# Optimization experiments

Measured on AMD Instinct MI355X. Metric: run time of the kernel, lower is better.

The kernel has to match this reference:

```python
import jax, jax.numpy as jnp
import numpy as np

EPS = 1e-5  # InstanceNorm3d default eps


def _conv3d(x, w, b):
    # x: [C, D, H, W]; w: [O, I, 3, 3, 3]; SAME padding (pw = k//2)
    y = jax.lax.conv_general_dilated(
        x[None], w, window_strides=(1, 1, 1), padding='SAME',
        dimension_numbers=('NCDHW', 'OIDHW', 'NCDHW'))[0]
    return y + b[:, None, None, None]


def _spade(x, ws, bs, wg, bg, wb, bb):
    # x: [C, D, H, W] single sample; per-class SPADE params
    mu = x.mean(axis=(1, 2, 3), keepdims=True)
    var = x.var(axis=(1, 2, 3), keepdims=True)  # biased var, as in InstanceNorm
    normalized = (x - mu) * jax.lax.rsqrt(var + EPS)
    actv = jax.nn.relu(_conv3d(x, ws, bs))
    gamma = _conv3d(actv, wg, bg)
    beta = _conv3d(actv, wb, bb)
    return normalized * (1.0 + gamma) + beta


def setup_inputs() -> dict:
    key = jax.random.key(0)
    ks = jax.random.split(key, 6)
    B, C, D = 8, 32, 48
    NC, NH = 4, 64  # num_classes, nhidden
    s = 0.05
    return {
        'x': jax.random.normal(ks[0], (B, C, D, D, D), jnp.float32),
        'y': jax.random.randint(ks[1], (B,), 0, NC),
        'Wshared': jax.random.normal(ks[2], (NC, NH, C, 3, 3, 3), jnp.float32) * s,
        'bshared': jnp.zeros((NC, NH), jnp.float32),
        'Wgamma': jax.random.normal(ks[3], (NC, C, NH, 3, 3, 3), jnp.float32) * s,
        'bgamma': jnp.zeros((NC, C), jnp.float32),
        'Wbeta': jax.random.normal(ks[4], (NC, C, NH, 3, 3, 3), jnp.float32) * s,
        'bbeta': jnp.zeros((NC, C), jnp.float32),
    }


def reference(x, y, Wshared, bshared, Wgamma, bgamma, Wbeta, bbeta):
    # Gather per-sample expert params by class index, then batch via vmap
    return jax.vmap(_spade)(x, Wshared[y], bshared[y], Wgamma[y], bgamma[y],
                            Wbeta[y], bbeta[y])
```

## Files before the change

kernel.cpp:

```cpp
#include <hip/hip_runtime.h>
#include <stdint.h>

#define V3 (48*48*48)
#define BATCH 8

typedef __bf16 bf16x8 __attribute__((ext_vector_type(8)));
typedef float  f32x4  __attribute__((ext_vector_type(4)));

__device__ __forceinline__ unsigned short f2bf(float f) {
  uint32_t u = __float_as_uint(f);
  u += 0x7fffu + ((u >> 16) & 1u);
  return (unsigned short)(u >> 16);
}

#define GLDS16(gp, lp)                                                         \
  __builtin_amdgcn_global_load_lds(                                            \
      (const __attribute__((address_space(1))) void*)(gp),                     \
      (__attribute__((address_space(3))) void*)(lp), 16, 0, 0)

__global__ __launch_bounds__(1024)
void stats_kernel(const float* __restrict__ x, float* __restrict__ mu,
                  float* __restrict__ rstd, float4* __restrict__ zpage) {
  if (blockIdx.x == 0 && threadIdx.x < 64) {
    float4 z; z.x = 0.f; z.y = 0.f; z.z = 0.f; z.w = 0.f;
    zpage[threadIdx.x] = z;
  }
  const int bc = blockIdx.x;
  const float4* p = reinterpret_cast<const float4*>(x + (size_t)bc * V3);
  float s = 0.f, s2 = 0.f;
  for (int i = threadIdx.x; i < V3 / 4; i += 1024) {
    float4 v = p[i];
    s  += (v.x + v.y) + (v.z + v.w);
    s2 += (v.x * v.x + v.y * v.y) + (v.z * v.z + v.w * v.w);
  }
  for (int o = 32; o; o >>= 1) { s += __shfl_down(s, o); s2 += __shfl_down(s2, o); }
  __shared__ float red[32];
  const int wave = threadIdx.x >> 6, lane = threadIdx.x & 63;
  if (lane == 0) { red[wave] = s; red[16 + wave] = s2; }
  __syncthreads();
  if (threadIdx.x == 0) {
    float S1 = 0.f, S2 = 0.f;
#pragma unroll
    for (int i = 0; i < 16; ++i) { S1 += red[i]; S2 += red[16 + i]; }
    float m = S1 / (float)V3;
    float var = S2 / (float)V3 - m * m;
    mu[bc] = m;
    rstd[bc] = rsqrtf(var + 1e-5f);
  }
}

__global__ __launch_bounds__(256)
void repack_kernel(const float* __restrict__ x, unsigned short* __restrict__ xcl) {
  const int bid = blockIdx.x;
  const int h = bid % 48;
  const int d = (bid / 48) % 48;
  const int b = bid / (48 * 48);
  __shared__ float tile[32][48];
  const float* src = x + (size_t)b * 32 * V3 + (size_t)(d * 48 + h) * 48;
  for (int i = threadIdx.x; i < 32 * 48; i += 256) {
    int c = i / 48, w = i - c * 48;
    tile[c][w] = src[(size_t)c * V3 + w];
  }
  __syncthreads();
  const int i = threadIdx.x;
  if (i < 48 * 4) {
    const int w = i >> 2, pp = i & 3;
    alignas(16) unsigned short pk[8];
#pragma unroll
    for (int j = 0; j < 8; ++j) pk[j] = f2bf(tile[pp * 8 + j][w]);
    *reinterpret_cast<uint4*>(
        &xcl[((size_t)b * V3 + (size_t)(d * 48 + h) * 48 + w) * 32 + pp * 8]) =
        *reinterpret_cast<const uint4*>(pk);
  }
}

__global__ __launch_bounds__(256)
void wprep_kernel(const int* __restrict__ y, const float* __restrict__ Wsh,
                  const float* __restrict__ Wg, const float* __restrict__ Wb,
                  unsigned short* __restrict__ w1, unsigned short* __restrict__ w23) {
  const int N1 = BATCH * 27 * 4 * 64 * 8;
  const int N2 = BATCH * 2 * 27 * 4 * 64 * 8;
  int idx = blockIdx.x * 256 + threadIdx.x;
  if (idx < N1) {
    const int j = idx & 7;
    const int lane = (idx >> 3) & 63;
    const int mt = (idx >> 9) & 3;
    const int tap = (idx >> 11) % 27;
    const int b = idx / (27 << 11);
    const int q = lane >> 4, n = lane & 15;
    const int cout = mt * 16 + n, cin = q * 8 + j;
    const int cls = y[b];
    w1[idx] = f2bf(Wsh[((size_t)((cls * 64 + cout) * 32 + cin)) * 27 + tap]);
  } else if (idx < N1 + N2) {
    const int t = idx - N1;
    const int b = t / 110592;
    const int r1 = t - b * 110592;
    const int kc = r1 / 55296;
    const int r2 = r1 - kc * 55296;
    const int tap = r2 >> 11;
    const int r3 = r2 & 2047;
    const int mt = r3 >> 9;
    const int lane = (r3 >> 3) & 63;
    const int j = r3 & 7;
    const int q = lane >> 4, n = lane & 15;
    const int cout = mt * 16 + n, cin = kc * 32 + q * 8 + j;
    const int cls = y[b];
    float v = (cout < 32) ? Wg[((size_t)((cls * 32 + cout) * 64 + cin)) * 27 + tap]
                          : Wb[((size_t)((cls * 32 + (cout - 32)) * 64 + cin)) * 27 + tap];
    w23[t] = f2bf(v);
  }
}


#define STAGE_K(K0, K1, SRC_EXPR)                                              \
  do {                                                                         \
    _Pragma("unroll") for (int k = (K0); k < (K1); ++k) {                      \
      const int j = tid + k * 256;                                             \
      if (k < 10 || tid < 32) {                                                \
        const int ld_ = j / 432;                                               \
        const int r = j - ld_ * 432;                                           \
        const int pp = r / 108;                                                \
        const int r2 = r - pp * 108;                                           \
        const int lh = r2 / 18;                                                \
        const int lw = r2 - lh * 18;                                           \
        const int d = d0 + ld_ - 1, h = h0 + lh - 1, w = w0 + lw - 1;          \
        const bool ok = (unsigned)d < 48u && (unsigned)h < 48u && (unsigned)w < 48u; \
        const void* gp = ok ? (const void*)(SRC_EXPR)                          \
                            : (const void*)((const char*)zpage + lane * 16);   \
        GLDS16(gp, &lds[(size_t)(j - lane) * 8]);                              \
      }                                                                        \
    }                                                                          \
  } while (0)

#define STAGE11(SRC_EXPR)                                                      \
  do {                                                                         \
    STAGE_K(0, 7, SRC_EXPR);                                                   \
    __builtin_amdgcn_sched_barrier(0);         \
    STAGE_K(7, 11, SRC_EXPR);                                                  \
  } while (0)

#define WAIT_VM(N)                                                             \
  asm volatile("s_waitcnt vmcnt(" #N ")" ::: "memory")

#define COMPUTE_TAPS_PF(T0, T1, WB)                                            \
  do {                                                                         \
    __builtin_amdgcn_s_setprio(1);                                             \
    _Pragma("unroll 1") for (int tap = (T0); tap < (T1); ++tap) {              \
      bf16x8 anxt[4];                                                          \
      _Pragma("unroll") for (int mt = 0; mt < 4; ++mt)                         \
        anxt[mt] = *reinterpret_cast<const bf16x8*>(                           \
            &(WB)[((tap + 1) * 4 + mt) * 512]);                                \
      const int dz_ = tap / 9, rr_ = tap - dz_ * 9;                            \
      const int dy_ = rr_ / 3, dx_ = rr_ - dy_ * 3;                            \
      const int vb_ = ((wave + dz_) * 4 + q) * 108 + dy_ * 18 + dx_ + n;       \
      bf16x8 bf[4];                                                            \
      _Pragma("unroll") for (int g = 0; g < 4; ++g)                            \
        bf[g] = *reinterpret_cast<const bf16x8*>(&lds[(size_t)(vb_ + g * 18) * 8]); \
      _Pragma("unroll") for (int g = 0; g < 4; ++g)                            \
        _Pragma("unroll") for (int mt = 0; mt < 4; ++mt)                       \
          acc[g][mt] = __builtin_amdgcn_mfma_f32_16x16x32_bf16(                \
              acur[mt], bf[g], acc[g][mt], 0, 0, 0);                           \
      _Pragma("unroll") for (int mt = 0; mt < 4; ++mt) acur[mt] = anxt[mt];    \
    }                                                                          \
    __builtin_amdgcn_s_setprio(0);                                             \
  } while (0)

#define COMPUTE_TAP26()                                                        \
  do {                                                                         \
    __builtin_amdgcn_s_setprio(1);                                             \
    const int vb_ = ((wave + 2) * 4 + q) * 108 + 2 * 18 + 2 + n;               \
    bf16x8 bf[4];                                                              \
    _Pragma("unroll") for (int g = 0; g < 4; ++g)                              \
      bf[g] = *reinterpret_cast<const bf16x8*>(&lds[(size_t)(vb_ + g * 18) * 8]); \
    _Pragma("unroll") for (int g = 0; g < 4; ++g)                              \
      _Pragma("unroll") for (int mt = 0; mt < 4; ++mt)                         \
        acc[g][mt] = __builtin_amdgcn_mfma_f32_16x16x32_bf16(                  \
            acur[mt], bf[g], acc[g][mt], 0, 0, 0);                             \
    __builtin_amdgcn_s_setprio(0);                                             \
  } while (0)

__global__ __launch_bounds__(256, 3)
void conv1_kernel(const unsigned short* __restrict__ xcl,
                  const unsigned short* __restrict__ w1,
                  const int* __restrict__ y, const float* __restrict__ bsh,
                  unsigned short* __restrict__ actv,
                  const float4* __restrict__ zpage) {
  const int d0 = (blockIdx.y / 12) * 4;
  const int h0 = (blockIdx.y % 12) * 4;
  const int w0 = blockIdx.x * 16;
  const int b = blockIdx.z;

  __shared__ unsigned short lds[2592 * 8];

  const int tid = threadIdx.x;
  const int lane = tid & 63;
  const int wave = tid >> 6;
  const int q = lane >> 4, n = lane & 15;

  const unsigned short* xb = xcl + (size_t)b * V3 * 32;
  STAGE11(xb + ((size_t)((d * 48 + h) * 48 + w)) * 32 + pp * 8);

  const unsigned short* wb = w1 + (size_t)b * 55296 + lane * 8;
  bf16x8 acur[4];
#pragma unroll
  for (int mt = 0; mt < 4; ++mt)
    acur[mt] = *reinterpret_cast<const bf16x8*>(&wb[mt * 512]);
  __builtin_amdgcn_sched_barrier(0);

  f32x4 acc[4][4];
#pragma unroll
  for (int g = 0; g < 4; ++g)
#pragma unroll
    for (int mt = 0; mt < 4; ++mt) acc[g][mt] = (f32x4){0.f, 0.f, 0.f, 0.f};

  WAIT_VM(7);
  __builtin_amdgcn_s_barrier();
  COMPUTE_TAPS_PF(0, 9, wb);
  WAIT_VM(4);
  __builtin_amdgcn_s_barrier();
  COMPUTE_TAPS_PF(9, 26, wb);
  COMPUTE_TAP26();

  const int cls = y[b];
  const int od = d0 + wave, ow = w0 + n;
#pragma unroll
  for (int g = 0; g < 4; ++g) {
    const int oh = h0 + g;
    const size_t vg = (size_t)(od * 48 + oh) * 48 + ow;
#pragma unroll
    for (int mt = 0; mt < 4; ++mt) {
      const int c0 = mt * 16 + q * 4;
      ushort4 pk;
      pk.x = f2bf(fmaxf(acc[g][mt][0] + bsh[cls * 64 + c0 + 0], 0.f));
      pk.y = f2bf(fmaxf(acc[g][mt][1] + bsh[cls * 64 + c0 + 1], 0.f));
      pk.z = f2bf(fmaxf(acc[g][mt][2] + bsh[cls * 64 + c0 + 2], 0.f));
      pk.w = f2bf(fmaxf(acc[g][mt][3] + bsh[cls * 64 + c0 + 3], 0.f));
      *reinterpret_cast<ushort4*>(&actv[((size_t)b * V3 + vg) * 64 + c0]) = pk;
    }
  }
}

__global__ __launch_bounds__(256, 3)
void conv2_kernel(const unsigned short* __restrict__ actv,
                  const unsigned short* __restrict__ w23,
                  const int* __restrict__ y, const float* __restrict__ bgm,
                  const float* __restrict__ bbt, const float* __restrict__ x,
                  const float* __restrict__ mu, const float* __restrict__ rstd,
                  float* __restrict__ out, const float4* __restrict__ zpage) {
  const int d0 = (blockIdx.y / 12) * 4;
  const int h0 = (blockIdx.y % 12) * 4;
  const int w0 = blockIdx.x * 16;
  const int b = blockIdx.z;

  __shared__ unsigned short lds[2592 * 8];

  const int tid = threadIdx.x;
  const int lane = tid & 63;
  const int wave = tid >> 6;
  const int q = lane >> 4, n = lane & 15;

  f32x4 acc[4][4];
#pragma unroll
  for (int g = 0; g < 4; ++g)
#pragma unroll
    for (int mt = 0; mt < 4; ++mt) acc[g][mt] = (f32x4){0.f, 0.f, 0.f, 0.f};

  const unsigned short* ab = actv + (size_t)b * V3 * 64;

  for (int kc = 0; kc < 2; ++kc) {
    if (kc) { __syncthreads(); }
    STAGE11(ab + ((size_t)((d * 48 + h) * 48 + w)) * 64 + kc * 32 + pp * 8);

    const unsigned short* wb =
        w23 + (size_t)b * 110592 + (size_t)kc * 55296 + lane * 8;
    bf16x8 acur[4];
#pragma unroll
    for (int mt = 0; mt < 4; ++mt)
      acur[mt] = *reinterpret_cast<const bf16x8*>(&wb[mt * 512]);
    __builtin_amdgcn_sched_barrier(0);

    WAIT_VM(7);
    __builtin_amdgcn_s_barrier();
    COMPUTE_TAPS_PF(0, 9, wb);
    WAIT_VM(4);
    __builtin_amdgcn_s_barrier();
    COMPUTE_TAPS_PF(9, 26, wb);
    COMPUTE_TAP26();
  }

  const int cls = y[b];
  const int od = d0 + wave, ow = w0 + n;
#pragma unroll
  for (int g = 0; g < 4; ++g) {
    const int oh = h0 + g;
    const size_t vg = (size_t)(od * 48 + oh) * 48 + ow;
#pragma unroll
    for (int mt = 0; mt < 2; ++mt) {
#pragma unroll
      for (int r = 0; r < 4; ++r) {
        const int c = mt * 16 + q * 4 + r;
        const float gamma = acc[g][mt][r] + bgm[cls * 32 + c];
        const float beta = acc[g][mt + 2][r] + bbt[cls * 32 + c];
        const size_t xi = (size_t)(b * 32 + c) * V3 + vg;
        const float xn = (x[xi] - mu[b * 32 + c]) * rstd[b * 32 + c];
        out[xi] = xn * (1.f + gamma) + beta;
      }
    }
  }
}

extern "C" void kernel_launch(void* const* d_in, const int* in_sizes, int n_in,
                              void* d_out, int out_size, void* d_ws, size_t ws_size,
                              hipStream_t stream) {
  const float* x = (const float*)d_in[0];
  const int* y = (const int*)d_in[1];
  const float* Wsh = (const float*)d_in[2];
  const float* bsh = (const float*)d_in[3];
  const float* Wg = (const float*)d_in[4];
  const float* bg = (const float*)d_in[5];
  const float* Wb = (const float*)d_in[6];
  const float* bb = (const float*)d_in[7];
  float* out = (float*)d_out;

  char* ws = (char*)d_ws;
  unsigned short* xcl  = (unsigned short*)(ws + 0);
  unsigned short* actv = (unsigned short*)(ws + 56623104);
  unsigned short* w1   = (unsigned short*)(ws + 169869312);
  unsigned short* w23  = (unsigned short*)(ws + 170754048);
  float* mu    = (float*)(ws + 172523520);
  float* rstd  = (float*)(ws + 172524544);
  float4* zpg  = (float4*)(ws + 172525568);

  stats_kernel<<<256, 1024, 0, stream>>>(x, mu, rstd, zpg);
  repack_kernel<<<BATCH * 48 * 48, 256, 0, stream>>>(x, xcl);
  wprep_kernel<<<(BATCH * 27 * 4 * 64 * 8 * 3 + 255) / 256, 256, 0, stream>>>(
      y, Wsh, Wg, Wb, w1, w23);

  dim3 grid(3, 144, BATCH);
  conv1_kernel<<<grid, 256, 0, stream>>>(xcl, w1, y, bsh, actv, zpg);
  conv2_kernel<<<grid, 256, 0, stream>>>(actv, w23, y, bg, bb, x, mu, rstd, out, zpg);
}
```

Baseline: 593.6 us.

## Reuse LDS B-fragments across dy taps by looping dx outer, dy inner

Restructures the tap loop so each (dz, dx) pass loads six LDS rows once and reuses them across the three dy taps through a sliding window (bf[g+dy]). This cuts LDS reads per tap from 4 fragments to 2 on average. The weight prefetch order is reworked to follow the new tap order, and the special last-tap block is folded into the loop. Launch bounds drop from 3 to 2 waves per SIMD to leave room for the extra registers, which may lower occupancy and latency hiding.

Measured after the change: 615.0 us. 1.04x slower.

```diff
diff --git a/kernel.cpp b/kernel.cpp
--- a/kernel.cpp
+++ b/kernel.cpp
@@ -142,44 +142,34 @@
 #define WAIT_VM(N)                                                             \
   asm volatile("s_waitcnt vmcnt(" #N ")" ::: "memory")
 
-#define COMPUTE_TAPS_PF(T0, T1, WB)                                            \
+#define COMPUTE_DZ(DZ, WB)                                                     \
   do {                                                                         \
-    __builtin_amdgcn_s_setprio(1);                                             \
-    _Pragma("unroll 1") for (int tap = (T0); tap < (T1); ++tap) {              \
-      bf16x8 anxt[4];                                                          \
-      _Pragma("unroll") for (int mt = 0; mt < 4; ++mt)                         \
-        anxt[mt] = *reinterpret_cast<const bf16x8*>(                           \
-            &(WB)[((tap + 1) * 4 + mt) * 512]);                                \
-      const int dz_ = tap / 9, rr_ = tap - dz_ * 9;                            \
-      const int dy_ = rr_ / 3, dx_ = rr_ - dy_ * 3;                            \
-      const int vb_ = ((wave + dz_) * 4 + q) * 108 + dy_ * 18 + dx_ + n;       \
-      bf16x8 bf[4];                                                            \
-      _Pragma("unroll") for (int g = 0; g < 4; ++g)                            \
-        bf[g] = *reinterpret_cast<const bf16x8*>(&lds[(size_t)(vb_ + g * 18) * 8]); \
-      _Pragma("unroll") for (int g = 0; g < 4; ++g)                            \
+    _Pragma("unroll 1") for (int dxi = 0; dxi < 3; ++dxi) {                    \
+      const int base_ = ((wave + (DZ)) * 4 + q) * 108 + dxi + n;               \
+      bf16x8 bf[6];                                                            \
+      _Pragma("unroll") for (int r = 0; r < 6; ++r)                            \
+        bf[r] = *reinterpret_cast<const bf16x8*>(                              \
+            &lds[(size_t)(base_ + r * 18) * 8]);                               \
+      __builtin_amdgcn_s_setprio(1);                                           \
+      _Pragma("unroll") for (int dy = 0; dy < 3; ++dy) {                       \
+        const int wn = (dy < 2) ? ((DZ) * 9 + (dy + 1) * 3 + dxi)              \
+                     : (dxi < 2 ? ((DZ) * 9 + dxi + 1)                         \
+                                : ((DZ) < 2 ? ((DZ) + 1) * 9 : 26));           \
+        bf16x8 anxt[4];                                                        \
         _Pragma("unroll") for (int mt = 0; mt < 4; ++mt)                       \
-          acc[g][mt] = __builtin_amdgcn_mfma_f32_16x16x32_bf16(                \
-              acur[mt], bf[g], acc[g][mt], 0, 0, 0);                           \
-      _Pragma("unroll") for (int mt = 0; mt < 4; ++mt) acur[mt] = anxt[mt];    \
+          anxt[mt] = *reinterpret_cast<const bf16x8*>(                         \
+              &(WB)[(wn * 4 + mt) * 512]);                                     \
+        _Pragma("unroll") for (int g = 0; g < 4; ++g)                          \
+          _Pragma("unroll") for (int mt = 0; mt < 4; ++mt)                     \
+            acc[g][mt] = __builtin_amdgcn_mfma_f32_16x16x32_bf16(              \
+                acur[mt], bf[g + dy], acc[g][mt], 0, 0, 0);                    \
+        _Pragma("unroll") for (int mt = 0; mt < 4; ++mt) acur[mt] = anxt[mt];  \
+      }                                                                        \
+      __builtin_amdgcn_s_setprio(0);                                           \
     }                                                                          \
-    __builtin_amdgcn_s_setprio(0);                                             \
   } while (0)
 
-#define COMPUTE_TAP26()                                                        \
-  do {                                                                         \
-    __builtin_amdgcn_s_setprio(1);                                             \
-    const int vb_ = ((wave + 2) * 4 + q) * 108 + 2 * 18 + 2 + n;               \
-    bf16x8 bf[4];                                                              \
-    _Pragma("unroll") for (int g = 0; g < 4; ++g)                              \
-      bf[g] = *reinterpret_cast<const bf16x8*>(&lds[(size_t)(vb_ + g * 18) * 8]); \
-    _Pragma("unroll") for (int g = 0; g < 4; ++g)                              \
-      _Pragma("unroll") for (int mt = 0; mt < 4; ++mt)                         \
-        acc[g][mt] = __builtin_amdgcn_mfma_f32_16x16x32_bf16(                  \
-            acur[mt], bf[g], acc[g][mt], 0, 0, 0);                             \
-    __builtin_amdgcn_s_setprio(0);                                             \
-  } while (0)
-
-__global__ __launch_bounds__(256, 3)
+__global__ __launch_bounds__(256, 2)
 void conv1_kernel(const unsigned short* __restrict__ xcl,
                   const unsigned short* __restrict__ w1,
                   const int* __restrict__ y, const float* __restrict__ bsh,
@@ -215,11 +205,11 @@
 
   WAIT_VM(7);
   __builtin_amdgcn_s_barrier();
-  COMPUTE_TAPS_PF(0, 9, wb);
+  COMPUTE_DZ(0, wb);
   WAIT_VM(4);
   __builtin_amdgcn_s_barrier();
-  COMPUTE_TAPS_PF(9, 26, wb);
-  COMPUTE_TAP26();
+  COMPUTE_DZ(1, wb);
+  COMPUTE_DZ(2, wb);
 
   const int cls = y[b];
   const int od = d0 + wave, ow = w0 + n;
@@ -240,7 +230,7 @@
   }
 }
 
-__global__ __launch_bounds__(256, 3)
+__global__ __launch_bounds__(256, 2)
 void conv2_kernel(const unsigned short* __restrict__ actv,
                   const unsigned short* __restrict__ w23,
                   const int* __restrict__ y, const float* __restrict__ bgm,
@@ -281,11 +271,11 @@
 
     WAIT_VM(7);
     __builtin_amdgcn_s_barrier();
-    COMPUTE_TAPS_PF(0, 9, wb);
+    COMPUTE_DZ(0, wb);
     WAIT_VM(4);
     __builtin_amdgcn_s_barrier();
-    COMPUTE_TAPS_PF(9, 26, wb);
-    COMPUTE_TAP26();
+    COMPUTE_DZ(1, wb);
+    COMPUTE_DZ(2, wb);
   }
 
   const int cls = y[b];
```
